# Performance work log

Measured on AMD Instinct MI355X. Metric: run time of the kernel, lower is better.

## Reference

```python
import jax, jax.numpy as jnp
import numpy as np
import math

N = 100000        # nodes
E = 3200000       # edges (avg degree 32)
DIN = 128         # in_features
DOUT = 64         # out_features
LAMDA = 0.5       # GCNII lambda
ALPHA = 0.1       # GCNII alpha
L = 1             # layer index


def setup_inputs() -> dict:
    key = jax.random.key(0)
    ks = jax.random.split(key, 6)
    x = jax.random.normal(ks[0], (N, DIN), dtype=jnp.float32)
    adj_rows = jnp.sort(jax.random.randint(ks[1], (E,), 0, N, dtype=jnp.int32))
    adj_cols = jax.random.randint(ks[2], (E,), 0, N, dtype=jnp.int32)
    adj_vals = jax.random.uniform(ks[3], (E,), dtype=jnp.float32)
    h0 = jax.random.normal(ks[4], (N, DOUT), dtype=jnp.float32)
    weight = jax.random.normal(ks[5], (DIN, DOUT), dtype=jnp.float32) * 0.02  # xavier-ish gain 0.02
    bias = jnp.zeros((1, DOUT), dtype=jnp.float32)
    return {"x": x, "adj_rows": adj_rows, "adj_cols": adj_cols,
            "adj_vals": adj_vals, "h0": h0, "weight": weight, "bias": bias}


def reference(x, adj_rows, adj_cols, adj_vals, h0, weight, bias):
    theta = math.log(LAMDA / L + 1)
    # dense projection: [N, DIN] @ [DIN, DOUT]
    xw = x @ weight
    # SpMM: hi[r] = sum_{e: rows[e]==r} vals[e] * xw[cols[e]]
    hi = jax.ops.segment_sum(adj_vals[:, None] * xw[adj_cols], adj_rows, num_segments=N)
    # non-variant GCNII combine
    support = (1.0 - ALPHA) * hi + ALPHA * h0
    r = support
    out = theta * support + (1.0 - theta) * r
    return out + bias
```

## Files before the change

### kernel.cpp

```cpp
#include <hip/hip_runtime.h>

#define N_NODES 100000
#define N_EDGES 3200000
#define DIN     128
#define DOUT    64

typedef unsigned short bf16_t;
typedef float f32x4 __attribute__((ext_vector_type(4)));

__device__ __forceinline__ bf16_t f32_to_bf16(float f) {
    union { float f; unsigned int u; } un; un.f = f;
    unsigned int u = un.u + 0x7fffu + ((un.u >> 16) & 1u);
    return (bf16_t)(u >> 16);
}
__device__ __forceinline__ float2 bf16x2_to_f32x2(unsigned int p) {
    union { unsigned int u; float f; } lo, hi;
    lo.u = p << 16;
    hi.u = p & 0xffff0000u;
    return make_float2(lo.f, hi.f);
}

#define UNPACK_FMA(ACC, G, VV)                                    \
    do {                                                          \
        const float2 _f0 = bf16x2_to_f32x2((G).x);                \
        const float2 _f1 = bf16x2_to_f32x2((G).y);                \
        const float2 _f2 = bf16x2_to_f32x2((G).z);                \
        const float2 _f3 = bf16x2_to_f32x2((G).w);                \
        ACC[0] += (VV) * _f0.x; ACC[1] += (VV) * _f0.y;           \
        ACC[2] += (VV) * _f1.x; ACC[3] += (VV) * _f1.y;           \
        ACC[4] += (VV) * _f2.x; ACC[5] += (VV) * _f2.y;           \
        ACC[6] += (VV) * _f3.x; ACC[7] += (VV) * _f3.y;           \
    } while (0)

#define MASKED_GROUP(ACC, EBASE)                                        \
    do {                                                                \
        const int   _ei = (EBASE) + grp;                                \
        const bool  _ok = _ei < end;                                    \
        const int   _ec = _ok ? _ei : (end - 1);                        \
        const int   _cc = cols[_ec];                                    \
        const float _vv = _ok ? vals[_ec] : 0.f;                        \
        const uint4 _g  = *(const uint4*)&xwb[_cc * DOUT + 8 * fq];     \
        UNPACK_FMA(ACC, _g, _vv);                                       \
    } while (0)

__global__ __launch_bounds__(256) void gemm_xw_bf16(const float* __restrict__ x,
                                                    const float* __restrict__ w,
                                                    bf16_t* __restrict__ xwb) {
    __shared__ float Xs[64][DIN];
    __shared__ float Ws[DIN][DOUT];

    const int tid = threadIdx.x;
    const int block_row = blockIdx.x * 64;

    {
        const float4* w4 = (const float4*)w;
        float4* ws4 = (float4*)Ws;
        for (int i = tid; i < DIN * DOUT / 4; i += 256)
            ws4[i] = w4[i];
    }
    for (int i = tid; i < 64 * DIN / 4; i += 256) {
        const int r  = i >> 5;
        const int k4 = i & 31;
        const int gr = block_row + r;
        float4 v = make_float4(0.f, 0.f, 0.f, 0.f);
        if (gr < N_NODES) v = ((const float4*)x)[gr * (DIN / 4) + k4];
        ((float4*)&Xs[r][0])[k4 ^ (r & 7)] = v;
    }
    __syncthreads();

    const int tx = tid & 15;
    const int ty = tid >> 4;

    float acc[4][4] = {};
#pragma unroll 2
    for (int k4 = 0; k4 < DIN / 4; ++k4) {
        float4 xr[4];
#pragma unroll
        for (int j = 0; j < 4; ++j) {
            const int r = ty * 4 + j;
            xr[j] = ((const float4*)&Xs[r][0])[k4 ^ (r & 7)];
        }
#pragma unroll
        for (int kk = 0; kk < 4; ++kk) {
            const float4 wv = ((const float4*)Ws)[(k4 * 4 + kk) * (DOUT / 4) + tx];
            const float xv0 = (kk == 0) ? xr[0].x : (kk == 1) ? xr[0].y : (kk == 2) ? xr[0].z : xr[0].w;
            const float xv1 = (kk == 0) ? xr[1].x : (kk == 1) ? xr[1].y : (kk == 2) ? xr[1].z : xr[1].w;
            const float xv2 = (kk == 0) ? xr[2].x : (kk == 1) ? xr[2].y : (kk == 2) ? xr[2].z : xr[2].w;
            const float xv3 = (kk == 0) ? xr[3].x : (kk == 1) ? xr[3].y : (kk == 2) ? xr[3].z : xr[3].w;
            acc[0][0] += xv0 * wv.x; acc[0][1] += xv0 * wv.y; acc[0][2] += xv0 * wv.z; acc[0][3] += xv0 * wv.w;
            acc[1][0] += xv1 * wv.x; acc[1][1] += xv1 * wv.y; acc[1][2] += xv1 * wv.z; acc[1][3] += xv1 * wv.w;
            acc[2][0] += xv2 * wv.x; acc[2][1] += xv2 * wv.y; acc[2][2] += xv2 * wv.z; acc[2][3] += xv2 * wv.w;
            acc[3][0] += xv3 * wv.x; acc[3][1] += xv3 * wv.y; acc[3][2] += xv3 * wv.z; acc[3][3] += xv3 * wv.w;
        }
    }

#pragma unroll
    for (int j = 0; j < 4; ++j) {
        const int gr = block_row + ty * 4 + j;
        if (gr < N_NODES) {
            const unsigned int p0 = (unsigned int)f32_to_bf16(acc[j][0]) |
                                    ((unsigned int)f32_to_bf16(acc[j][1]) << 16);
            const unsigned int p1 = (unsigned int)f32_to_bf16(acc[j][2]) |
                                    ((unsigned int)f32_to_bf16(acc[j][3]) << 16);
            uint2 pk; pk.x = p0; pk.y = p1;
            *(uint2*)&xwb[gr * DOUT + tx * 4] = pk;
        }
    }
}

__global__ __launch_bounds__(256) void build_row_ptr(const int* __restrict__ rows,
                                                     int* __restrict__ row_ptr) {
    const int e = blockIdx.x * blockDim.x + threadIdx.x;
    if (e >= N_EDGES) return;
    const int cur  = rows[e];
    const int prev = (e == 0) ? -1 : rows[e - 1];
    for (int r = prev + 1; r <= cur; ++r) row_ptr[r] = e;
    if (e == N_EDGES - 1) {
        for (int r = cur + 1; r <= N_NODES; ++r) row_ptr[r] = N_EDGES;
    }
}

__global__ __launch_bounds__(256) void spmm_combine(const bf16_t* __restrict__ xwb,
                                                    const int*    __restrict__ row_ptr,
                                                    const int*    __restrict__ cols,
                                                    const float*  __restrict__ vals,
                                                    const float*  __restrict__ h0,
                                                    const float*  __restrict__ bias,
                                                    float* __restrict__ out) {
    const int wid  = (blockIdx.x * blockDim.x + threadIdx.x) >> 6;
    const int lane = threadIdx.x & 63;
    if (wid >= N_NODES) return;

    const int grp = lane >> 3;
    const int fq  = lane & 7;

    const int row   = __builtin_amdgcn_readfirstlane(wid);
    const int start = __builtin_amdgcn_readfirstlane(row_ptr[row]);
    const int end   = __builtin_amdgcn_readfirstlane(row_ptr[row + 1]);

    const f32x4 ha = __builtin_nontemporal_load((const f32x4*)&h0[row * DOUT + 8 * fq]);
    const f32x4 hb = __builtin_nontemporal_load((const f32x4*)&h0[row * DOUT + 8 * fq + 4]);
    const f32x4 ba = *(const f32x4*)&bias[8 * fq];
    const f32x4 bb = *(const f32x4*)&bias[8 * fq + 4];

    float accA[8] = {};
    float accB[8] = {};

    if (start < end) {
        int e = start;
        for (; e + 32 <= end; e += 32) {
            const int   c0 = cols[e      + grp];
            const int   c1 = cols[e + 8  + grp];
            const int   c2 = cols[e + 16 + grp];
            const int   c3 = cols[e + 24 + grp];
            const float v0 = vals[e      + grp];
            const float v1 = vals[e + 8  + grp];
            const float v2 = vals[e + 16 + grp];
            const float v3 = vals[e + 24 + grp];
            const uint4 g0 = *(const uint4*)&xwb[c0 * DOUT + 8 * fq];
            const uint4 g1 = *(const uint4*)&xwb[c1 * DOUT + 8 * fq];
            const uint4 g2 = *(const uint4*)&xwb[c2 * DOUT + 8 * fq];
            const uint4 g3 = *(const uint4*)&xwb[c3 * DOUT + 8 * fq];
            UNPACK_FMA(accA, g0, v0);
            UNPACK_FMA(accB, g1, v1);
            UNPACK_FMA(accA, g2, v2);
            UNPACK_FMA(accB, g3, v3);
        }
        for (; e < end; e += 16) {
            MASKED_GROUP(accA, e);
            if (e + 8 < end) MASKED_GROUP(accB, e + 8);
        }
    }

    float s0, s1, s2, s3, s4, s5, s6, s7;
#define REDUCE_J(SJ, J)                                  \
    do {                                                 \
        float _t = accA[J] + accB[J];                    \
        _t += __shfl_xor(_t, 8, 64);                     \
        _t += __shfl_xor(_t, 16, 64);                    \
        _t += __shfl_xor(_t, 32, 64);                    \
        SJ = _t;                                         \
    } while (0)
    REDUCE_J(s0, 0); REDUCE_J(s1, 1); REDUCE_J(s2, 2); REDUCE_J(s3, 3);
    REDUCE_J(s4, 4); REDUCE_J(s5, 5); REDUCE_J(s6, 6); REDUCE_J(s7, 7);
#undef REDUCE_J

    if (grp == 0) {
        f32x4 ra, rb;
        ra.x = 0.9f * s0 + 0.1f * ha.x + ba.x;
        ra.y = 0.9f * s1 + 0.1f * ha.y + ba.y;
        ra.z = 0.9f * s2 + 0.1f * ha.z + ba.z;
        ra.w = 0.9f * s3 + 0.1f * ha.w + ba.w;
        rb.x = 0.9f * s4 + 0.1f * hb.x + bb.x;
        rb.y = 0.9f * s5 + 0.1f * hb.y + bb.y;
        rb.z = 0.9f * s6 + 0.1f * hb.z + bb.z;
        rb.w = 0.9f * s7 + 0.1f * hb.w + bb.w;
        __builtin_nontemporal_store(ra, (f32x4*)&out[row * DOUT + 8 * fq]);
        __builtin_nontemporal_store(rb, (f32x4*)&out[row * DOUT + 8 * fq + 4]);
    }
}

extern "C" void kernel_launch(void* const* d_in, const int* in_sizes, int n_in,
                              void* d_out, int out_size, void* d_ws, size_t ws_size,
                              hipStream_t stream) {
    const float* x    = (const float*)d_in[0];
    const int*   rows = (const int*)  d_in[1];
    const int*   cols = (const int*)  d_in[2];
    const float* vals = (const float*)d_in[3];
    const float* h0   = (const float*)d_in[4];
    const float* w    = (const float*)d_in[5];
    const float* bias = (const float*)d_in[6];
    float* out = (float*)d_out;

    bf16_t* xwb = (bf16_t*)d_ws;
    const size_t xw_bytes = (size_t)N_NODES * DOUT * sizeof(bf16_t);
    int* row_ptr = (int*)((char*)d_ws + xw_bytes);

    gemm_xw_bf16<<<(N_NODES + 63) / 64, 256, 0, stream>>>(x, w, xwb);
    build_row_ptr<<<(N_EDGES + 255) / 256, 256, 0, stream>>>(rows, row_ptr);
    spmm_combine<<<(N_NODES * DOUT + 255) / 256, 256, 0, stream>>>(
        xwb, row_ptr, cols, vals, h0, bias, out);
}
```

Before: 110.3 us.

## Use MFMA bf16 GEMM, merge row-pointer build into it, process two rows per wave

The fp32 FMA GEMM becomes a bf16 MFMA 16x16x32 GEMM with a swizzled, transposed weight tile in shared memory. The row_ptr construction is folded into the same launch as extra blocks, removing one kernel launch. The SpMM now gives each wave two rows with interleaved gathers, so more loads are in flight per wave. In exchange, x and W are rounded to bf16 before the multiply, which lowers precision, and the output stores are scattered 2-byte writes.

```diff
diff --git a/kernel.cpp b/kernel.cpp
--- a/kernel.cpp
+++ b/kernel.cpp
@@ -4,14 +4,20 @@
 #define N_EDGES 3200000
 #define DIN     128
 #define DOUT    64
+#define GEMM_BLOCKS 1563
+#define RP_BLOCKS   12500
 
 typedef unsigned short bf16_t;
-typedef float f32x4 __attribute__((ext_vector_type(4)));
+typedef float f32x4  __attribute__((ext_vector_type(4)));
+typedef short bf16x8 __attribute__((ext_vector_type(8)));
 
 __device__ __forceinline__ bf16_t f32_to_bf16(float f) {
     union { float f; unsigned int u; } un; un.f = f;
     unsigned int u = un.u + 0x7fffu + ((un.u >> 16) & 1u);
     return (bf16_t)(u >> 16);
+}
+__device__ __forceinline__ unsigned int pack2(float lo, float hi) {
+    return (unsigned int)f32_to_bf16(lo) | ((unsigned int)f32_to_bf16(hi) << 16);
 }
 __device__ __forceinline__ float2 bf16x2_to_f32x2(unsigned int p) {
     union { unsigned int u; float f; } lo, hi;
@@ -32,171 +38,231 @@
         ACC[6] += (VV) * _f3.x; ACC[7] += (VV) * _f3.y;           \
     } while (0)
 
-#define MASKED_GROUP(ACC, EBASE)                                        \
-    do {                                                                \
-        const int   _ei = (EBASE) + grp;                                \
-        const bool  _ok = _ei < end;                                    \
-        const int   _ec = _ok ? _ei : (end - 1);                        \
-        const int   _cc = cols[_ec];                                    \
-        const float _vv = _ok ? vals[_ec] : 0.f;                        \
-        const uint4 _g  = *(const uint4*)&xwb[_cc * DOUT + 8 * fq];     \
-        UNPACK_FMA(ACC, _g, _vv);                                       \
-    } while (0)
-
-__global__ __launch_bounds__(256) void gemm_xw_bf16(const float* __restrict__ x,
-                                                    const float* __restrict__ w,
-                                                    bf16_t* __restrict__ xwb) {
-    __shared__ float Xs[64][DIN];
-    __shared__ float Ws[DIN][DOUT];
-
+#define MASKED_GROUP(ACC, EBASE, END)                                       \
+    do {                                                                    \
+        const int   _ei = (EBASE) + grp;                                    \
+        const bool  _ok = _ei < (END);                                      \
+        const int   _ec = _ok ? _ei : ((END) - 1);                          \
+        const int   _cc = cols[_ec];                                        \
+        const float _vv = _ok ? vals[_ec] : 0.f;                            \
+        const uint4 _g  = *(const uint4*)&xwb[(size_t)_cc * DOUT + 8 * fq]; \
+        UNPACK_FMA(ACC, _g, _vv);                                           \
+    } while (0)
+
+#define OCTET4(ACC, P)                                                      \
+    do {                                                                    \
+        const int   _c0 = cols[(P) + grp];                                  \
+        const int   _c1 = cols[(P) + 8  + grp];                             \
+        const int   _c2 = cols[(P) + 16 + grp];                             \
+        const int   _c3 = cols[(P) + 24 + grp];                             \
+        const float _v0 = vals[(P) + grp];                                  \
+        const float _v1 = vals[(P) + 8  + grp];                             \
+        const float _v2 = vals[(P) + 16 + grp];                             \
+        const float _v3 = vals[(P) + 24 + grp];                             \
+        const uint4 _g0 = *(const uint4*)&xwb[(size_t)_c0 * DOUT + 8 * fq]; \
+        const uint4 _g1 = *(const uint4*)&xwb[(size_t)_c1 * DOUT + 8 * fq]; \
+        const uint4 _g2 = *(const uint4*)&xwb[(size_t)_c2 * DOUT + 8 * fq]; \
+        const uint4 _g3 = *(const uint4*)&xwb[(size_t)_c3 * DOUT + 8 * fq]; \
+        UNPACK_FMA(ACC, _g0, _v0);                                          \
+        UNPACK_FMA(ACC, _g1, _v1);                                          \
+        UNPACK_FMA(ACC, _g2, _v2);                                          \
+        UNPACK_FMA(ACC, _g3, _v3);                                          \
+    } while (0)
+
+__global__ __launch_bounds__(256) void gemm_rowptr(const float* __restrict__ x,
+                                                   const float* __restrict__ w,
+                                                   const int*   __restrict__ rows,
+                                                   bf16_t* __restrict__ xwb,
+                                                   int* __restrict__ row_ptr) {
+    __shared__ unsigned short Xs[64][DIN];
+    __shared__ unsigned short Wt[DOUT][DIN];
+
+    const int bid = blockIdx.x;
     const int tid = threadIdx.x;
-    const int block_row = blockIdx.x * 64;
+
+    if (bid >= GEMM_BLOCKS) {
+        const int e = (bid - GEMM_BLOCKS) * 256 + tid;
+        if (e < N_EDGES) {
+            const int cur  = rows[e];
+            const int prev = (e == 0) ? -1 : rows[e - 1];
+            for (int r = prev + 1; r <= cur; ++r) row_ptr[r] = e;
+            if (e == N_EDGES - 1)
+                for (int r = cur + 1; r <= N_NODES; ++r) row_ptr[r] = N_EDGES;
+        }
+        return;
+    }
+
+    const int block_row = bid * 64;
 
     {
         const float4* w4 = (const float4*)w;
-        float4* ws4 = (float4*)Ws;
-        for (int i = tid; i < DIN * DOUT / 4; i += 256)
-            ws4[i] = w4[i];
-    }
-    for (int i = tid; i < 64 * DIN / 4; i += 256) {
-        const int r  = i >> 5;
-        const int k4 = i & 31;
+#pragma unroll
+        for (int i = 0; i < 8; ++i) {
+            const int f4 = i * 256 + tid;
+            const float4 v = w4[f4];
+            const int base = f4 * 4;
+            const int k = base >> 6;
+            const int n = base & 63;
+            Wt[n + 0][(((k >> 3) ^ ((n + 0) & 7)) << 3) | (k & 7)] = f32_to_bf16(v.x);
+            Wt[n + 1][(((k >> 3) ^ ((n + 1) & 7)) << 3) | (k & 7)] = f32_to_bf16(v.y);
+            Wt[n + 2][(((k >> 3) ^ ((n + 2) & 7)) << 3) | (k & 7)] = f32_to_bf16(v.z);
+            Wt[n + 3][(((k >> 3) ^ ((n + 3) & 7)) << 3) | (k & 7)] = f32_to_bf16(v.w);
+        }
+    }
+    {
+        const int r = tid >> 2;
+        const int q = tid & 3;
         const int gr = block_row + r;
-        float4 v = make_float4(0.f, 0.f, 0.f, 0.f);
-        if (gr < N_NODES) v = ((const float4*)x)[gr * (DIN / 4) + k4];
-        ((float4*)&Xs[r][0])[k4 ^ (r & 7)] = v;
+        const float4* xp = (const float4*)&x[(size_t)gr * DIN + q * 32];
+        const bool ok = gr < N_NODES;
+#pragma unroll
+        for (int ci = 0; ci < 4; ++ci) {
+            float4 a = make_float4(0.f, 0.f, 0.f, 0.f), b = a;
+            if (ok) { a = xp[2 * ci]; b = xp[2 * ci + 1]; }
+            uint4 pk;
+            pk.x = pack2(a.x, a.y);
+            pk.y = pack2(a.z, a.w);
+            pk.z = pack2(b.x, b.y);
+            pk.w = pack2(b.z, b.w);
+            const int c = q * 4 + ci;
+            *(uint4*)&Xs[r][(c ^ (r & 7)) << 3] = pk;
+        }
     }
     __syncthreads();
 
-    const int tx = tid & 15;
-    const int ty = tid >> 4;
-
-    float acc[4][4] = {};
-#pragma unroll 2
-    for (int k4 = 0; k4 < DIN / 4; ++k4) {
-        float4 xr[4];
-#pragma unroll
-        for (int j = 0; j < 4; ++j) {
-            const int r = ty * 4 + j;
-            xr[j] = ((const float4*)&Xs[r][0])[k4 ^ (r & 7)];
-        }
-#pragma unroll
-        for (int kk = 0; kk < 4; ++kk) {
-            const float4 wv = ((const float4*)Ws)[(k4 * 4 + kk) * (DOUT / 4) + tx];
-            const float xv0 = (kk == 0) ? xr[0].x : (kk == 1) ? xr[0].y : (kk == 2) ? xr[0].z : xr[0].w;
-            const float xv1 = (kk == 0) ? xr[1].x : (kk == 1) ? xr[1].y : (kk == 2) ? xr[1].z : xr[1].w;
-            const float xv2 = (kk == 0) ? xr[2].x : (kk == 1) ? xr[2].y : (kk == 2) ? xr[2].z : xr[2].w;
-            const float xv3 = (kk == 0) ? xr[3].x : (kk == 1) ? xr[3].y : (kk == 2) ? xr[3].z : xr[3].w;
-            acc[0][0] += xv0 * wv.x; acc[0][1] += xv0 * wv.y; acc[0][2] += xv0 * wv.z; acc[0][3] += xv0 * wv.w;
-            acc[1][0] += xv1 * wv.x; acc[1][1] += xv1 * wv.y; acc[1][2] += xv1 * wv.z; acc[1][3] += xv1 * wv.w;
-            acc[2][0] += xv2 * wv.x; acc[2][1] += xv2 * wv.y; acc[2][2] += xv2 * wv.z; acc[2][3] += xv2 * wv.w;
-            acc[3][0] += xv3 * wv.x; acc[3][1] += xv3 * wv.y; acc[3][2] += xv3 * wv.z; acc[3][3] += xv3 * wv.w;
-        }
-    }
-
-#pragma unroll
-    for (int j = 0; j < 4; ++j) {
-        const int gr = block_row + ty * 4 + j;
-        if (gr < N_NODES) {
-            const unsigned int p0 = (unsigned int)f32_to_bf16(acc[j][0]) |
-                                    ((unsigned int)f32_to_bf16(acc[j][1]) << 16);
-            const unsigned int p1 = (unsigned int)f32_to_bf16(acc[j][2]) |
-                                    ((unsigned int)f32_to_bf16(acc[j][3]) << 16);
-            uint2 pk; pk.x = p0; pk.y = p1;
-            *(uint2*)&xwb[gr * DOUT + tx * 4] = pk;
-        }
-    }
-}
-
-__global__ __launch_bounds__(256) void build_row_ptr(const int* __restrict__ rows,
-                                                     int* __restrict__ row_ptr) {
-    const int e = blockIdx.x * blockDim.x + threadIdx.x;
-    if (e >= N_EDGES) return;
-    const int cur  = rows[e];
-    const int prev = (e == 0) ? -1 : rows[e - 1];
-    for (int r = prev + 1; r <= cur; ++r) row_ptr[r] = e;
-    if (e == N_EDGES - 1) {
-        for (int r = cur + 1; r <= N_NODES; ++r) row_ptr[r] = N_EDGES;
-    }
-}
-
-__global__ __launch_bounds__(256) void spmm_combine(const bf16_t* __restrict__ xwb,
-                                                    const int*    __restrict__ row_ptr,
-                                                    const int*    __restrict__ cols,
-                                                    const float*  __restrict__ vals,
-                                                    const float*  __restrict__ h0,
-                                                    const float*  __restrict__ bias,
-                                                    float* __restrict__ out) {
+    const int wv_ = tid >> 6;
+    const int l   = tid & 63;
+    const int lr  = l & 15;
+    const int hi  = l >> 4;
+    const int arow = wv_ * 16 + lr;
+
+    f32x4 acc0 = {0.f, 0.f, 0.f, 0.f};
+    f32x4 acc1 = acc0, acc2 = acc0, acc3 = acc0;
+#pragma unroll
+    for (int s = 0; s < 4; ++s) {
+        const int kc = s * 4 + hi;
+        const bf16x8 a  = *(const bf16x8*)&Xs[arow][(kc ^ (arow & 7)) << 3];
+        const int bc = (kc ^ (lr & 7)) << 3;
+        const bf16x8 b0 = *(const bf16x8*)&Wt[lr     ][bc];
+        const bf16x8 b1 = *(const bf16x8*)&Wt[16 + lr][bc];
+        const bf16x8 b2 = *(const bf16x8*)&Wt[32 + lr][bc];
+        const bf16x8 b3 = *(const bf16x8*)&Wt[48 + lr][bc];
+        acc0 = __builtin_amdgcn_mfma_f32_16x16x32_bf16(a, b0, acc0, 0, 0, 0);
+        acc1 = __builtin_amdgcn_mfma_f32_16x16x32_bf16(a, b1, acc1, 0, 0, 0);
+        acc2 = __builtin_amdgcn_mfma_f32_16x16x32_bf16(a, b2, acc2, 0, 0, 0);
+        acc3 = __builtin_amdgcn_mfma_f32_16x16x32_bf16(a, b3, acc3, 0, 0, 0);
+    }
+
+#pragma unroll
+    for (int reg = 0; reg < 4; ++reg) {
+        const int grow = block_row + wv_ * 16 + hi * 4 + reg;
+        if (grow < N_NODES) {
+            bf16_t* o = &xwb[(size_t)grow * DOUT + lr];
+            o[0]  = f32_to_bf16(acc0[reg]);
+            o[16] = f32_to_bf16(acc1[reg]);
+            o[32] = f32_to_bf16(acc2[reg]);
+            o[48] = f32_to_bf16(acc3[reg]);
+        }
+    }
+}
+
+__global__ __launch_bounds__(256) void spmm2(const bf16_t* __restrict__ xwb,
+                                             const int*    __restrict__ row_ptr,
+                                             const int*    __restrict__ cols,
+                                             const float*  __restrict__ vals,
+                                             const float*  __restrict__ h0,
+                                             const float*  __restrict__ bias,
+                                             float* __restrict__ out) {
     const int wid  = (blockIdx.x * blockDim.x + threadIdx.x) >> 6;
     const int lane = threadIdx.x & 63;
-    if (wid >= N_NODES) return;
+    const int r0 = wid << 1;
+    if (r0 >= N_NODES) return;
 
     const int grp = lane >> 3;
     const int fq  = lane & 7;
-
-    const int row   = __builtin_amdgcn_readfirstlane(wid);
-    const int start = __builtin_amdgcn_readfirstlane(row_ptr[row]);
-    const int end   = __builtin_amdgcn_readfirstlane(row_ptr[row + 1]);
-
-    const f32x4 ha = __builtin_nontemporal_load((const f32x4*)&h0[row * DOUT + 8 * fq]);
-    const f32x4 hb = __builtin_nontemporal_load((const f32x4*)&h0[row * DOUT + 8 * fq + 4]);
+    const bool has1 = (r0 + 1) < N_NODES;
+
+    const int s0 = __builtin_amdgcn_readfirstlane(row_ptr[r0]);
+    const int m0 = __builtin_amdgcn_readfirstlane(row_ptr[r0 + 1]);
+    const int e1 = has1 ? __builtin_amdgcn_readfirstlane(row_ptr[r0 + 2]) : m0;
+
+    const int rsel = (grp == 1 && has1) ? (r0 + 1) : r0;
+    const f32x4 ha = __builtin_nontemporal_load((const f32x4*)&h0[(size_t)rsel * DOUT + 8 * fq]);
+    const f32x4 hb = __builtin_nontemporal_load((const f32x4*)&h0[(size_t)rsel * DOUT + 8 * fq + 4]);
     const f32x4 ba = *(const f32x4*)&bias[8 * fq];
     const f32x4 bb = *(const f32x4*)&bias[8 * fq + 4];
 
     float accA[8] = {};
     float accB[8] = {};
-
-    if (start < end) {
-        int e = start;
-        for (; e + 32 <= end; e += 32) {
-            const int   c0 = cols[e      + grp];
-            const int   c1 = cols[e + 8  + grp];
-            const int   c2 = cols[e + 16 + grp];
-            const int   c3 = cols[e + 24 + grp];
-            const float v0 = vals[e      + grp];
-            const float v1 = vals[e + 8  + grp];
-            const float v2 = vals[e + 16 + grp];
-            const float v3 = vals[e + 24 + grp];
-            const uint4 g0 = *(const uint4*)&xwb[c0 * DOUT + 8 * fq];
-            const uint4 g1 = *(const uint4*)&xwb[c1 * DOUT + 8 * fq];
-            const uint4 g2 = *(const uint4*)&xwb[c2 * DOUT + 8 * fq];
-            const uint4 g3 = *(const uint4*)&xwb[c3 * DOUT + 8 * fq];
-            UNPACK_FMA(accA, g0, v0);
-            UNPACK_FMA(accB, g1, v1);
-            UNPACK_FMA(accA, g2, v2);
-            UNPACK_FMA(accB, g3, v3);
-        }
-        for (; e < end; e += 16) {
-            MASKED_GROUP(accA, e);
-            if (e + 8 < end) MASKED_GROUP(accB, e + 8);
-        }
-    }
-
-    float s0, s1, s2, s3, s4, s5, s6, s7;
-#define REDUCE_J(SJ, J)                                  \
+    int p0 = s0, p1 = m0;
+
+    while (p0 + 16 <= m0 && p1 + 16 <= e1) {
+        const int   c00 = cols[p0 + grp];
+        const int   c01 = cols[p0 + 8 + grp];
+        const int   c10 = cols[p1 + grp];
+        const int   c11 = cols[p1 + 8 + grp];
+        const float v00 = vals[p0 + grp];
+        const float v01 = vals[p0 + 8 + grp];
+        const float v10 = vals[p1 + grp];
+        const float v11 = vals[p1 + 8 + grp];
+        const uint4 g00 = *(const uint4*)&xwb[(size_t)c00 * DOUT + 8 * fq];
+        const uint4 g01 = *(const uint4*)&xwb[(size_t)c01 * DOUT + 8 * fq];
+        const uint4 g10 = *(const uint4*)&xwb[(size_t)c10 * DOUT + 8 * fq];
+        const uint4 g11 = *(const uint4*)&xwb[(size_t)c11 * DOUT + 8 * fq];
+        UNPACK_FMA(accA, g00, v00);
+        UNPACK_FMA(accA, g01, v01);
+        UNPACK_FMA(accB, g10, v10);
+        UNPACK_FMA(accB, g11, v11);
+        p0 += 16; p1 += 16;
+    }
+    for (; p0 + 32 <= m0; p0 += 32) OCTET4(accA, p0);
+    for (; p0 < m0; p0 += 16) {
+        MASKED_GROUP(accA, p0, m0);
+        if (p0 + 8 < m0) MASKED_GROUP(accA, p0 + 8, m0);
+    }
+    for (; p1 + 32 <= e1; p1 += 32) OCTET4(accB, p1);
+    for (; p1 < e1; p1 += 16) {
+        MASKED_GROUP(accB, p1, e1);
+        if (p1 + 8 < e1) MASKED_GROUP(accB, p1 + 8, e1);
+    }
+
+#define RED(ACC, J, S)                                   \
     do {                                                 \
-        float _t = accA[J] + accB[J];                    \
+        float _t = ACC[J];                               \
         _t += __shfl_xor(_t, 8, 64);                     \
         _t += __shfl_xor(_t, 16, 64);                    \
         _t += __shfl_xor(_t, 32, 64);                    \
-        SJ = _t;                                         \
-    } while (0)
-    REDUCE_J(s0, 0); REDUCE_J(s1, 1); REDUCE_J(s2, 2); REDUCE_J(s3, 3);
-    REDUCE_J(s4, 4); REDUCE_J(s5, 5); REDUCE_J(s6, 6); REDUCE_J(s7, 7);
-#undef REDUCE_J
-
-    if (grp == 0) {
+        S = _t;                                          \
+    } while (0)
+    float a0, a1, a2, a3, a4, a5, a6, a7;
+    float b0, b1, b2, b3, b4, b5, b6, b7;
+    RED(accA, 0, a0); RED(accA, 1, a1); RED(accA, 2, a2); RED(accA, 3, a3);
+    RED(accA, 4, a4); RED(accA, 5, a5); RED(accA, 6, a6); RED(accA, 7, a7);
+    RED(accB, 0, b0); RED(accB, 1, b1); RED(accB, 2, b2); RED(accB, 3, b3);
+    RED(accB, 4, b4); RED(accB, 5, b5); RED(accB, 6, b6); RED(accB, 7, b7);
+#undef RED
+
+    if (grp == 0 || (grp == 1 && has1)) {
+        const bool g1 = (grp == 1);
+        const float t0 = g1 ? b0 : a0;
+        const float t1 = g1 ? b1 : a1;
+        const float t2 = g1 ? b2 : a2;
+        const float t3 = g1 ? b3 : a3;
+        const float t4 = g1 ? b4 : a4;
+        const float t5 = g1 ? b5 : a5;
+        const float t6 = g1 ? b6 : a6;
+        const float t7 = g1 ? b7 : a7;
         f32x4 ra, rb;
-        ra.x = 0.9f * s0 + 0.1f * ha.x + ba.x;
-        ra.y = 0.9f * s1 + 0.1f * ha.y + ba.y;
-        ra.z = 0.9f * s2 + 0.1f * ha.z + ba.z;
-        ra.w = 0.9f * s3 + 0.1f * ha.w + ba.w;
-        rb.x = 0.9f * s4 + 0.1f * hb.x + bb.x;
-        rb.y = 0.9f * s5 + 0.1f * hb.y + bb.y;
-        rb.z = 0.9f * s6 + 0.1f * hb.z + bb.z;
-        rb.w = 0.9f * s7 + 0.1f * hb.w + bb.w;
-        __builtin_nontemporal_store(ra, (f32x4*)&out[row * DOUT + 8 * fq]);
-        __builtin_nontemporal_store(rb, (f32x4*)&out[row * DOUT + 8 * fq + 4]);
+        ra.x = 0.9f * t0 + 0.1f * ha.x + ba.x;
+        ra.y = 0.9f * t1 + 0.1f * ha.y + ba.y;
+        ra.z = 0.9f * t2 + 0.1f * ha.z + ba.z;
+        ra.w = 0.9f * t3 + 0.1f * ha.w + ba.w;
+        rb.x = 0.9f * t4 + 0.1f * hb.x + bb.x;
+        rb.y = 0.9f * t5 + 0.1f * hb.y + bb.y;
+        rb.z = 0.9f * t6 + 0.1f * hb.z + bb.z;
+        rb.w = 0.9f * t7 + 0.1f * hb.w + bb.w;
+        __builtin_nontemporal_store(ra, (f32x4*)&out[(size_t)rsel * DOUT + 8 * fq]);
+        __builtin_nontemporal_store(rb, (f32x4*)&out[(size_t)rsel * DOUT + 8 * fq + 4]);
     }
 }
 
@@ -216,8 +282,7 @@
     const size_t xw_bytes = (size_t)N_NODES * DOUT * sizeof(bf16_t);
     int* row_ptr = (int*)((char*)d_ws + xw_bytes);
 
-    gemm_xw_bf16<<<(N_NODES + 63) / 64, 256, 0, stream>>>(x, w, xwb);
-    build_row_ptr<<<(N_EDGES + 255) / 256, 256, 0, stream>>>(rows, row_ptr);
-    spmm_combine<<<(N_NODES * DOUT + 255) / 256, 256, 0, stream>>>(
+    gemm_rowptr<<<GEMM_BLOCKS + RP_BLOCKS, 256, 0, stream>>>(x, w, rows, xwb, row_ptr);
+    spmm2<<<(N_NODES / 2 * 64 + 255) / 256, 256, 0, stream>>>(
         xwb, row_ptr, cols, vals, h0, bias, out);
 }
```

After: 97.66 us. 1.13x faster.
